# Kernel tuning notes

Hardware: AMD Instinct MI355X
Metric: run time of the kernel (lower is better)

## Reference

```python
import jax, jax.numpy as jnp
import numpy as np

B, T, I, H = 8192, 2048, 2, 20


def setup_inputs() -> dict:
    key = jax.random.key(0)
    ks = jax.random.split(key, 7)
    s = 1.0 / np.sqrt(H).astype(np.float32)  # PyTorch RNN/Linear init bound
    u = lambda k, shp: jax.random.uniform(k, shp, minval=-s, maxval=s, dtype=jnp.float32)
    return {
        "x": jax.random.normal(ks[0], (B, T, I), dtype=jnp.float32),
        "W_ih": u(ks[1], (H, I)),
        "W_hh": u(ks[2], (H, H)),
        "b_ih": u(ks[3], (H,)),
        "b_hh": u(ks[4], (H,)),
        "fc_w": u(ks[5], (1, H)),
        "fc_b": u(ks[6], (1,)),
    }


def reference(x, W_ih, W_hh, b_ih, b_hh, fc_w, fc_b):
    # x: [B, T, I] (batch_first). Precompute input contribution for all steps.
    # xw: [T, B, H] -- time-major for lax.scan
    xw = jnp.einsum("bti,hi->tbh", x, W_ih) + b_ih + b_hh
    h0 = jnp.zeros((x.shape[0], H), dtype=x.dtype)

    def step(h, xw_t):
        h_new = jnp.tanh(xw_t + h @ W_hh.T)  # tanh-RNN recurrence
        return h_new, None

    hT, _ = jax.lax.scan(step, h0, xw)
    out = hT @ fc_w.T + fc_b          # fc on last timestep: [B, 1]
    h_state = hT[None]                # [1, B, H] like nn.RNN's h_n
    return out, h_state
```

## Files before the change

### kernel.cpp

```cpp
#include <hip/hip_runtime.h>


#define T_STEPS 2048
#define B_ROWS  8192
#define NCHUNK  (T_STEPS / 8)

#define XOR1_CTRL 0xB1
#define XOR2_CTRL 0x4E
#define MIR7_CTRL 0x141

typedef float f32x2 __attribute__((ext_vector_type(2)));

__device__ __forceinline__ float tanh_fast(float a) {
    float e = __builtin_amdgcn_exp2f(a * 2.8853900817779268f);
    float r = __builtin_amdgcn_rcpf(e + 1.0f);
    return fmaf(-2.0f, r, 1.0f);
}

template <int CTRL>
__device__ __forceinline__ float dpp_t(float old_, float src) {
    return __int_as_float(__builtin_amdgcn_update_dpp(
        __float_as_int(old_), __float_as_int(src), CTRL, 0xF, 0xF, false));
}

template <int CTRL>
__device__ __forceinline__ float dpp_full(float v) {
    return __int_as_float(__builtin_amdgcn_update_dpp(
        0, __float_as_int(v), CTRL, 0xF, 0xF, true));
}

__device__ __forceinline__ void pk_fma_acc(f32x2& c, f32x2 a, f32x2 b) {
    asm("v_pk_fma_f32 %0, %1, %2, %0" : "+v"(c) : "v"(a), "v"(b));
}
__device__ __forceinline__ f32x2 pk_fma3(f32x2 a, f32x2 b, f32x2 c) {
    f32x2 d;
    asm("v_pk_fma_f32 %0, %1, %2, %3" : "=v"(d) : "v"(a), "v"(b), "v"(c));
    return d;
}

__global__ __launch_bounds__(64, 1) void rnn_fused(
    const float* __restrict__ x,
    const float* __restrict__ W_ih,
    const float* __restrict__ W_hh,
    const float* __restrict__ b_ih,
    const float* __restrict__ b_hh,
    const float* __restrict__ fc_w,
    const float* __restrict__ fc_b,
    float* __restrict__ out)
{
    const int lane = threadIdx.x & 63;
    const int g    = lane & 7;
    const int r    = lane >> 3;
    const int row  = blockIdx.x * 8 + r;

    const int M[8] = {0, 7, 1, 6, 2, 5, 3, 4};

    f32x2 W2[3][12];
    f32x2 wiP[3], bP[3];
    float fcw[3];
#pragma unroll
    for (int jj = 0; jj < 3; ++jj) {
        const int j = 3 * g + jj;
        const bool v = (j < 20);
#pragma unroll
        for (int p = 0; p < 12; ++p) {
            float wv[2];
#pragma unroll
            for (int h = 0; h < 2; ++h) {
                const int slot = 2 * p + h;
                const int k = 3 * (g ^ M[slot / 3]) + (slot % 3);
                wv[h] = (v && k < 20) ? W_hh[j * 20 + k] : 0.0f;
            }
            W2[jj][p].x = wv[0];
            W2[jj][p].y = wv[1];
        }
        wiP[jj].x = v ? W_ih[j * 2 + 0] : 0.0f;
        wiP[jj].y = v ? W_ih[j * 2 + 1] : 0.0f;
        bP[jj].x  = v ? (b_ih[j] + b_hh[j]) : 0.0f;
        bP[jj].y  = 0.0f;
        fcw[jj]   = v ? fc_w[j] : 0.0f;
    }

    f32x2 hp[12];
#pragma unroll
    for (int i = 0; i < 12; ++i) { hp[i].x = 0.0f; hp[i].y = 0.0f; }

    auto step = [&](float x0, float x1) {
        f32x2 xp; xp.x = x0; xp.y = x1;
        f32x2 c0 = pk_fma3(xp, wiP[0], bP[0]);
        f32x2 c1 = pk_fma3(xp, wiP[1], bP[1]);
        f32x2 c2 = pk_fma3(xp, wiP[2], bP[2]);
#pragma unroll
        for (int p = 0; p < 12; ++p) {
            pk_fma_acc(c0, hp[p], W2[0][p]);
            pk_fma_acc(c1, hp[p], W2[1][p]);
            pk_fma_acc(c2, hp[p], W2[2][p]);
        }
        const float h0 = tanh_fast(c0.x + c0.y);
        const float h1 = tanh_fast(c1.x + c1.y);
        const float h2 = tanh_fast(c2.x + c2.y);
        hp[0].x = h0; hp[0].y = h1; hp[1].x = h2;
        hp[1].y = dpp_t<MIR7_CTRL>(hp[1].y, hp[0].x);
        hp[2].x = dpp_t<MIR7_CTRL>(hp[2].x, hp[0].y);
        hp[2].y = dpp_t<MIR7_CTRL>(hp[2].y, hp[1].x);
        hp[3].x = dpp_t<XOR1_CTRL>(hp[3].x, hp[0].x);
        hp[3].y = dpp_t<XOR1_CTRL>(hp[3].y, hp[0].y);
        hp[4].x = dpp_t<XOR1_CTRL>(hp[4].x, hp[1].x);
        hp[4].y = dpp_t<XOR1_CTRL>(hp[4].y, hp[1].y);
        hp[5].x = dpp_t<XOR1_CTRL>(hp[5].x, hp[2].x);
        hp[5].y = dpp_t<XOR1_CTRL>(hp[5].y, hp[2].y);
        hp[6].x  = dpp_t<XOR2_CTRL>(hp[6].x,  hp[0].x);
        hp[6].y  = dpp_t<XOR2_CTRL>(hp[6].y,  hp[0].y);
        hp[7].x  = dpp_t<XOR2_CTRL>(hp[7].x,  hp[1].x);
        hp[7].y  = dpp_t<XOR2_CTRL>(hp[7].y,  hp[1].y);
        hp[8].x  = dpp_t<XOR2_CTRL>(hp[8].x,  hp[2].x);
        hp[8].y  = dpp_t<XOR2_CTRL>(hp[8].y,  hp[2].y);
        hp[9].x  = dpp_t<XOR2_CTRL>(hp[9].x,  hp[3].x);
        hp[9].y  = dpp_t<XOR2_CTRL>(hp[9].y,  hp[3].y);
        hp[10].x = dpp_t<XOR2_CTRL>(hp[10].x, hp[4].x);
        hp[10].y = dpp_t<XOR2_CTRL>(hp[10].y, hp[4].y);
        hp[11].x = dpp_t<XOR2_CTRL>(hp[11].x, hp[5].x);
        hp[11].y = dpp_t<XOR2_CTRL>(hp[11].y, hp[5].y);
    };

    const float4* xq = (const float4*)(x + (size_t)row * (T_STEPS * 2));
    float4 q[4], qn[4];
#pragma unroll
    for (int i = 0; i < 4; ++i) q[i] = xq[i];

#pragma unroll 1
    for (int c = 0; c < NCHUNK; c += 2) {
        const int c1 = c + 1;
        const int c2 = (c + 2 < NCHUNK) ? (c + 2) : c1;
#pragma unroll
        for (int i = 0; i < 4; ++i) qn[i] = xq[4 * c1 + i];

        step(q[0].x, q[0].y); step(q[0].z, q[0].w);
        step(q[1].x, q[1].y); step(q[1].z, q[1].w);
        step(q[2].x, q[2].y); step(q[2].z, q[2].w);
        step(q[3].x, q[3].y); step(q[3].z, q[3].w);

#pragma unroll
        for (int i = 0; i < 4; ++i) q[i] = xq[4 * c2 + i];

        step(qn[0].x, qn[0].y); step(qn[0].z, qn[0].w);
        step(qn[1].x, qn[1].y); step(qn[1].z, qn[1].w);
        step(qn[2].x, qn[2].y); step(qn[2].z, qn[2].w);
        step(qn[3].x, qn[3].y); step(qn[3].z, qn[3].w);
    }

    {
        const int j0 = 3 * g;
        float* hs = out + B_ROWS + (size_t)row * 20;
        if (j0 + 0 < 20) hs[j0 + 0] = hp[0].x;
        if (j0 + 1 < 20) hs[j0 + 1] = hp[0].y;
        if (j0 + 2 < 20) hs[j0 + 2] = hp[1].x;
    }
    {
        float p = hp[0].x * fcw[0];
        p = fmaf(hp[0].y, fcw[1], p);
        p = fmaf(hp[1].x, fcw[2], p);
        p += dpp_full<XOR1_CTRL>(p);
        p += dpp_full<XOR2_CTRL>(p);
        p += dpp_full<MIR7_CTRL>(p);
        if (g == 0) out[row] = p + fc_b[0];
    }
}

extern "C" void kernel_launch(void* const* d_in, const int* in_sizes, int n_in,
                              void* d_out, int out_size, void* d_ws, size_t ws_size,
                              hipStream_t stream) {
    const float* x    = (const float*)d_in[0];
    const float* W_ih = (const float*)d_in[1];
    const float* W_hh = (const float*)d_in[2];
    const float* b_ih = (const float*)d_in[3];
    const float* b_hh = (const float*)d_in[4];
    const float* fc_w = (const float*)d_in[5];
    const float* fc_b = (const float*)d_in[6];
    float* out = (float*)d_out;

    rnn_fused<<<1024, 64, 0, stream>>>(x, W_ih, W_hh, b_ih, b_hh, fc_w, fc_b, out);
}
```

Measured before the change: 545.2 us.

## Exchange hidden state through LDS instead of DPP lane shuffles

Each lane writes its three new hidden values to a per-row shared-memory slot and reads back the full 24-entry row with vector loads, replacing the chain of DPP broadcasts. The recurrent weights are loaded in natural column order to match. This removes the many DPP move instructions per step, but it puts LDS write/read latency on the serial per-timestep critical path and relies on in-order LDS within a single wave.

New measurement: 568.4 us. 1.04x slower.

```diff
diff --git a/kernel.cpp b/kernel.cpp
--- a/kernel.cpp
+++ b/kernel.cpp
@@ -9,18 +9,14 @@
 #define XOR2_CTRL 0x4E
 #define MIR7_CTRL 0x141
 
+#define ROW_F 28
+
 typedef float f32x2 __attribute__((ext_vector_type(2)));
 
 __device__ __forceinline__ float tanh_fast(float a) {
     float e = __builtin_amdgcn_exp2f(a * 2.8853900817779268f);
     float r = __builtin_amdgcn_rcpf(e + 1.0f);
     return fmaf(-2.0f, r, 1.0f);
-}
-
-template <int CTRL>
-__device__ __forceinline__ float dpp_t(float old_, float src) {
-    return __int_as_float(__builtin_amdgcn_update_dpp(
-        __float_as_int(old_), __float_as_int(src), CTRL, 0xF, 0xF, false));
 }
 
 template <int CTRL>
@@ -53,7 +49,7 @@
     const int r    = lane >> 3;
     const int row  = blockIdx.x * 8 + r;
 
-    const int M[8] = {0, 7, 1, 6, 2, 5, 3, 4};
+    __shared__ float hsm[8 * ROW_F];
 
     f32x2 W2[3][12];
     f32x2 wiP[3], bP[3];
@@ -64,15 +60,9 @@
         const bool v = (j < 20);
 #pragma unroll
         for (int p = 0; p < 12; ++p) {
-            float wv[2];
-#pragma unroll
-            for (int h = 0; h < 2; ++h) {
-                const int slot = 2 * p + h;
-                const int k = 3 * (g ^ M[slot / 3]) + (slot % 3);
-                wv[h] = (v && k < 20) ? W_hh[j * 20 + k] : 0.0f;
-            }
-            W2[jj][p].x = wv[0];
-            W2[jj][p].y = wv[1];
+            const int k0 = 2 * p, k1 = 2 * p + 1;
+            W2[jj][p].x = (v && k0 < 20) ? W_hh[j * 20 + k0] : 0.0f;
+            W2[jj][p].y = (v && k1 < 20) ? W_hh[j * 20 + k1] : 0.0f;
         }
         wiP[jj].x = v ? W_ih[j * 2 + 0] : 0.0f;
         wiP[jj].y = v ? W_ih[j * 2 + 1] : 0.0f;
@@ -81,46 +71,34 @@
         fcw[jj]   = v ? fc_w[j] : 0.0f;
     }
 
-    f32x2 hp[12];
+    float*       hw   = &hsm[r * ROW_F + 3 * g];
+    const float4* hr4 = (const float4*)&hsm[r * ROW_F];
+
+    float h0 = 0.0f, h1 = 0.0f, h2 = 0.0f;
+    float4 hq[6];
+
+    hw[0] = 0.0f; hw[1] = 0.0f; hw[2] = 0.0f;
 #pragma unroll
-    for (int i = 0; i < 12; ++i) { hp[i].x = 0.0f; hp[i].y = 0.0f; }
+    for (int i = 0; i < 6; ++i) hq[i] = hr4[i];
 
     auto step = [&](float x0, float x1) {
         f32x2 xp; xp.x = x0; xp.y = x1;
         f32x2 c0 = pk_fma3(xp, wiP[0], bP[0]);
         f32x2 c1 = pk_fma3(xp, wiP[1], bP[1]);
         f32x2 c2 = pk_fma3(xp, wiP[2], bP[2]);
+        const f32x2* hp = (const f32x2*)hq;
 #pragma unroll
         for (int p = 0; p < 12; ++p) {
             pk_fma_acc(c0, hp[p], W2[0][p]);
             pk_fma_acc(c1, hp[p], W2[1][p]);
             pk_fma_acc(c2, hp[p], W2[2][p]);
         }
-        const float h0 = tanh_fast(c0.x + c0.y);
-        const float h1 = tanh_fast(c1.x + c1.y);
-        const float h2 = tanh_fast(c2.x + c2.y);
-        hp[0].x = h0; hp[0].y = h1; hp[1].x = h2;
-        hp[1].y = dpp_t<MIR7_CTRL>(hp[1].y, hp[0].x);
-        hp[2].x = dpp_t<MIR7_CTRL>(hp[2].x, hp[0].y);
-        hp[2].y = dpp_t<MIR7_CTRL>(hp[2].y, hp[1].x);
-        hp[3].x = dpp_t<XOR1_CTRL>(hp[3].x, hp[0].x);
-        hp[3].y = dpp_t<XOR1_CTRL>(hp[3].y, hp[0].y);
-        hp[4].x = dpp_t<XOR1_CTRL>(hp[4].x, hp[1].x);
-        hp[4].y = dpp_t<XOR1_CTRL>(hp[4].y, hp[1].y);
-        hp[5].x = dpp_t<XOR1_CTRL>(hp[5].x, hp[2].x);
-        hp[5].y = dpp_t<XOR1_CTRL>(hp[5].y, hp[2].y);
-        hp[6].x  = dpp_t<XOR2_CTRL>(hp[6].x,  hp[0].x);
-        hp[6].y  = dpp_t<XOR2_CTRL>(hp[6].y,  hp[0].y);
-        hp[7].x  = dpp_t<XOR2_CTRL>(hp[7].x,  hp[1].x);
-        hp[7].y  = dpp_t<XOR2_CTRL>(hp[7].y,  hp[1].y);
-        hp[8].x  = dpp_t<XOR2_CTRL>(hp[8].x,  hp[2].x);
-        hp[8].y  = dpp_t<XOR2_CTRL>(hp[8].y,  hp[2].y);
-        hp[9].x  = dpp_t<XOR2_CTRL>(hp[9].x,  hp[3].x);
-        hp[9].y  = dpp_t<XOR2_CTRL>(hp[9].y,  hp[3].y);
-        hp[10].x = dpp_t<XOR2_CTRL>(hp[10].x, hp[4].x);
-        hp[10].y = dpp_t<XOR2_CTRL>(hp[10].y, hp[4].y);
-        hp[11].x = dpp_t<XOR2_CTRL>(hp[11].x, hp[5].x);
-        hp[11].y = dpp_t<XOR2_CTRL>(hp[11].y, hp[5].y);
+        h0 = tanh_fast(c0.x + c0.y);
+        h1 = tanh_fast(c1.x + c1.y);
+        h2 = tanh_fast(c2.x + c2.y);
+        hw[0] = h0; hw[1] = h1; hw[2] = h2;
+#pragma unroll
+        for (int i = 0; i < 6; ++i) hq[i] = hr4[i];
     };
 
     const float4* xq = (const float4*)(x + (size_t)row * (T_STEPS * 2));
@@ -152,14 +130,14 @@
     {
         const int j0 = 3 * g;
         float* hs = out + B_ROWS + (size_t)row * 20;
-        if (j0 + 0 < 20) hs[j0 + 0] = hp[0].x;
-        if (j0 + 1 < 20) hs[j0 + 1] = hp[0].y;
-        if (j0 + 2 < 20) hs[j0 + 2] = hp[1].x;
+        if (j0 + 0 < 20) hs[j0 + 0] = h0;
+        if (j0 + 1 < 20) hs[j0 + 1] = h1;
+        if (j0 + 2 < 20) hs[j0 + 2] = h2;
     }
     {
-        float p = hp[0].x * fcw[0];
-        p = fmaf(hp[0].y, fcw[1], p);
-        p = fmaf(hp[1].x, fcw[2], p);
+        float p = h0 * fcw[0];
+        p = fmaf(h1, fcw[1], p);
+        p = fmaf(h2, fcw[2], p);
         p += dpp_full<XOR1_CTRL>(p);
         p += dpp_full<XOR2_CTRL>(p);
         p += dpp_full<MIR7_CTRL>(p);
```
